# Performance work log

Hardware: AMD Instinct MI355X
Metric: run time of the kernel (lower is better)

The kernel has to match this reference:

```python
import jax, jax.numpy as jnp
import numpy as np

B, N, T = 1, 1024, 2048   # batch, graph nodes, timesteps
E, K = 16384, 32          # edges, causal kernel taps


def setup_inputs() -> dict:
    key = jax.random.key(0)
    k1, k2, k3, k4 = jax.random.split(key, 4)
    x = jax.random.normal(k1, (B, N, T), dtype=jnp.float32)
    # per-edge causal impulse-response kernels (aggregator(g) output)
    kernel = jax.random.normal(k2, (E, K), dtype=jnp.float32) * 0.1
    src = jax.random.randint(k3, (E,), 0, N)
    dst = jax.random.randint(k4, (E,), 0, N)
    return {"x": x, "kernel": kernel, "src": src, "dst": dst}


def reference(x, kernel, src, dst):
    # Block-sparse causal conv over the edge list:
    #   y_e[b, t] = sum_k kernel[e, k] * x[b, src_e, t - k]   (causal)
    #   out[b, n, t] = x[b, n, t] + sum_{e: dst_e = n} y_e[b, t]
    # (residual applied because g.include_index_diag is False)
    xs = x[:, src, :]                      # [B, E, T] gather upstream signals
    rhs = kernel[:, None, ::-1]            # [E, 1, K] flipped -> true causal conv
    y = jax.lax.conv_general_dilated(
        xs, rhs,
        window_strides=(1,),
        padding=[(K - 1, 0)],              # left-pad: strictly causal
        dimension_numbers=("NCW", "OIW", "NCW"),
        feature_group_count=E,             # one independent kernel per edge
    )                                      # [B, E, T]
    agg = jax.ops.segment_sum(jnp.swapaxes(y, 0, 1), dst, num_segments=N)  # [N, B, T]
    return x + jnp.swapaxes(agg, 0, 1)     # [B, N, T]
```

## Files before the change

kernel.cpp:

```cpp
#include <hip/hip_runtime.h>
#include <hip/hip_bf16.h>

#define TT  2048
#define KK  32
#define NN  1024
#define EE  16384
#define CAP 64
#define RS  2080

typedef short short8 __attribute__((ext_vector_type(8)));
typedef float f32x4  __attribute__((ext_vector_type(4)));

__device__ short g_xbf[NN * RS];

__device__ __forceinline__ short f2bf(float f) {
    __hip_bfloat16 h = __float2bfloat16(f);
    return __builtin_bit_cast(short, h);
}

__device__ __forceinline__ void gload_lds16(const short* g, short* l) {
    __builtin_amdgcn_global_load_lds(
        (const __attribute__((address_space(1))) void*)(const void*)(g),
        (__attribute__((address_space(3))) void*)(void*)(l), 16, 0, 0);
}

__global__ __launch_bounds__(256) void cvt_kernel(const float* __restrict__ x,
                                                  int* __restrict__ cnt) {
    const int bid = blockIdx.x, tid = threadIdx.x;
    if (bid < NN) {
        const float4* xr = (const float4*)(x + (size_t)bid * TT);
        const float4 u = xr[2 * tid], v = xr[2 * tid + 1];
        short8 h;
        h[0]=f2bf(u.x); h[1]=f2bf(u.y); h[2]=f2bf(u.z); h[3]=f2bf(u.w);
        h[4]=f2bf(v.x); h[5]=f2bf(v.y); h[6]=f2bf(v.z); h[7]=f2bf(v.w);
        *(short8*)&g_xbf[(size_t)bid * RS + 32 + 8 * tid] = h;
        if (tid < 4) {
            short8 z; z[0]=0;z[1]=0;z[2]=0;z[3]=0;z[4]=0;z[5]=0;z[6]=0;z[7]=0;
            *(short8*)&g_xbf[(size_t)bid * RS + 8 * tid] = z;
        }
    } else {
        ((int4*)cnt)[tid] = make_int4(0, 0, 0, 0);
    }
}

__global__ __launch_bounds__(256) void csr_kernel(const int* __restrict__ src,
                                                  const int* __restrict__ dst,
                                                  int* __restrict__ cnt,
                                                  unsigned* __restrict__ slots) {
    const int e = blockIdx.x * 256 + threadIdx.x;
    const int d = dst[e];
    const int p = atomicAdd(&cnt[d], 1);
    if (p < CAP) slots[(size_t)d * CAP + p] = ((unsigned)src[e] << 14) | (unsigned)e;
}

__global__ __launch_bounds__(128, 2) void lti_kernel(
    const float*    __restrict__ x,
    const float*    __restrict__ kern,
    const int*      __restrict__ cnt,
    const unsigned* __restrict__ slots,
    float*          __restrict__ out)
{
    const int n   = blockIdx.x;
    const int tid = threadIdx.x;
    const int pw  = tid >> 6;
    const int ln  = tid & 63;
    const int c   = ln & 15, g = ln >> 4;
    const int D   = 16 * c + 8 * g;

    __shared__ __align__(16) short xs_all[2][3][RS];
    __shared__ __align__(16) short kt_all[2][8][72];
    __shared__ __align__(16) float red[TT];
    __shared__ unsigned bl[CAP];

    short (*xsb)[RS] = xs_all[pw];
    short (*kt)[72]  = kt_all[pw];

    short8 z8; z8[0]=0;z8[1]=0;z8[2]=0;z8[3]=0;z8[4]=0;z8[5]=0;z8[6]=0;z8[7]=0;

    {
        short8* kz = (short8*)&kt[0][0];
        kz[ln] = z8;
        if (ln < 8) kz[64 + ln] = z8;
    }
    if (tid < CAP) bl[tid] = slots[(size_t)n * CAP + tid];
    int L = cnt[n]; if (L > CAP) L = CAP;
    __syncthreads();

    const int M = (L - pw + 1) >> 1;
    #define IDX(I) (pw + 2 * (I))

    f32x4 acc[8];
    #pragma unroll
    for (int s = 0; s < 8; ++s) { acc[s][0]=0.f; acc[s][1]=0.f; acc[s][2]=0.f; acc[s][3]=0.f; }

    float4 tr0, tr1, tr2;

    const int a_ = c & 7;
    const int s1 = ((a_ + 1) & 7) + 15 - c + 8 * g;

    #define ISSUE(S, P)                                                                \
    {                                                                                  \
        const unsigned sv = bl[P];                                                     \
        const int e0 = __builtin_amdgcn_readfirstlane((int)(sv & 16383u));             \
        const int s0 = __builtin_amdgcn_readfirstlane((int)(sv >> 14));                \
        const short* rb = g_xbf + (size_t)s0 * RS;                                     \
        gload_lds16(rb + 8 * ln,        &xsb[S][0]);                                   \
        gload_lds16(rb + 8 * ln + 512,  &xsb[S][512]);                                 \
        gload_lds16(rb + 8 * ln + 1024, &xsb[S][1024]);                                \
        gload_lds16(rb + 8 * ln + 1536, &xsb[S][1536]);                                \
        if (ln < 4) gload_lds16(rb + 8 * ln + 2048, &xsb[S][2048]);                    \
        tr##S = *(const float4*)(kern + ((size_t)e0 << 5) + 4 * (ln & 7));             \
    }

    #define COMMIT(S)                                                                  \
    {                                                                                  \
        const int a2 = ln >> 3, pad = (a2 + 1) & 7, mb = 4 * (ln & 7);                 \
        kt[a2][pad + 47 - mb] = f2bf(tr##S.x);                                         \
        kt[a2][pad + 46 - mb] = f2bf(tr##S.y);                                         \
        kt[a2][pad + 45 - mb] = f2bf(tr##S.z);                                         \
        kt[a2][pad + 44 - mb] = f2bf(tr##S.w);                                         \
    }

    #define COMPUTE(S)                                                                 \
    {                                                                                  \
        const short8 b1 = *(const short8*)&kt[a_][s1];                                 \
        short8 b2 = *(const short8*)&kt[a_][s1 + 16];                                  \
        if (g < 2) b2 = z8;                              \
        _Pragma("unroll")                                                              \
        for (int s = 0; s < 8; ++s) {                                                  \
            const short8 a1  = *(const short8*)&xsb[S][256 * s + D];                   \
            const short8 a2v = *(const short8*)&xsb[S][256 * s + D + 16];              \
            acc[s] = __builtin_amdgcn_mfma_f32_16x16x32_bf16(a1,  b1, acc[s], 0,0,0);  \
            acc[s] = __builtin_amdgcn_mfma_f32_16x16x32_bf16(a2v, b2, acc[s], 0,0,0);  \
        }                                                                              \
    }

    #define BODY(SC, SN, I)                                                            \
    if ((I) < M) {                                                                     \
        __builtin_amdgcn_sched_barrier(0);                                             \
        if ((I) + 2 < M) ISSUE(SN, IDX((I) + 2));                                      \
        const int rem = M - (I);                                                       \
        if (rem >= 3)      { asm volatile("s_waitcnt vmcnt(12)" ::: "memory"); }       \
        else if (rem == 2) { asm volatile("s_waitcnt vmcnt(6)"  ::: "memory"); }       \
        else               { asm volatile("s_waitcnt vmcnt(0)"  ::: "memory"); }       \
        __builtin_amdgcn_sched_barrier(0);                                             \
        COMMIT(SC);                                                                    \
        COMPUTE(SC);                                                                   \
    }

    if (M > 0) ISSUE(0, IDX(0));
    if (M > 1) ISSUE(1, IDX(1));
    for (int i = 0; i < M; i += 3) {
        BODY(0, 2, i);
        BODY(1, 0, i + 1);
        BODY(2, 1, i + 2);
    }

    if (pw == 1) {
        #pragma unroll
        for (int s = 0; s < 8; ++s)
            #pragma unroll
            for (int qd = 0; qd < 4; ++qd)
                red[256 * s + 64 * g + 16 * qd + c] = acc[s][qd];
    }
    __syncthreads();
    if (pw == 0) {
        const float* xr  = x   + (size_t)n * TT;
        float*       orw = out + (size_t)n * TT;
        #pragma unroll
        for (int s = 0; s < 8; ++s) {
            #pragma unroll
            for (int qd = 0; qd < 4; ++qd) {
                const int ta = 256 * s + 64 * g + 16 * qd + c;
                orw[ta] = xr[ta] + acc[s][qd] + red[ta];
            }
        }
    }
    #undef IDX
    #undef ISSUE
    #undef COMMIT
    #undef COMPUTE
    #undef BODY
}

extern "C" void kernel_launch(void* const* d_in, const int* in_sizes, int n_in,
                              void* d_out, int out_size, void* d_ws, size_t ws_size,
                              hipStream_t stream) {
    const float* x    = (const float*)d_in[0];
    const float* kern = (const float*)d_in[1];
    const int*   src  = (const int*)d_in[2];
    const int*   dst  = (const int*)d_in[3];
    float*       out  = (float*)d_out;

    int*      cnt   = (int*)d_ws;
    unsigned* slots = (unsigned*)((char*)d_ws + 4096);

    cvt_kernel<<<dim3(NN + 1), dim3(256), 0, stream>>>(x, cnt);
    csr_kernel<<<dim3(EE / 256), dim3(256), 0, stream>>>(src, dst, cnt, slots);
    lti_kernel<<<dim3(NN), dim3(128), 0, stream>>>(x, kern, cnt, slots, out);
}
```

Baseline: 34.72 us.

## Quantize signals and kernels to int8 and use i8 MFMA with per-edge scales

Replaces the bf16 conversion of x with per-row symmetric int8 quantization, and quantizes each edge's kernel to int8 in the CSR build pass. A combined per-slot scale is precomputed. The conv now uses mfma_i32_16x16x32_i8 and rescales into float accumulators per edge. This halves the bytes gathered per edge and the LDS footprint, but adds per-edge int-to-float conversions and loses accuracy relative to bf16, which may exceed tolerance.

```diff
diff --git a/kernel.cpp b/kernel.cpp
--- a/kernel.cpp
+++ b/kernel.cpp
@@ -8,17 +8,14 @@
 #define CAP 64
 #define RS  2080
 
-typedef short short8 __attribute__((ext_vector_type(8)));
-typedef float f32x4  __attribute__((ext_vector_type(4)));
-
-__device__ short g_xbf[NN * RS];
-
-__device__ __forceinline__ short f2bf(float f) {
-    __hip_bfloat16 h = __float2bfloat16(f);
-    return __builtin_bit_cast(short, h);
-}
-
-__device__ __forceinline__ void gload_lds16(const short* g, short* l) {
+typedef int   int4v __attribute__((ext_vector_type(4)));
+typedef float f32x4 __attribute__((ext_vector_type(4)));
+
+__device__ __align__(16) char  g_xi8[NN * RS];
+__device__ __align__(16) char  g_ki8[EE * KK];
+__device__ float g_xs[NN];
+
+__device__ __forceinline__ void gload_lds16(const char* g, char* l) {
     __builtin_amdgcn_global_load_lds(
         (const __attribute__((address_space(1))) void*)(const void*)(g),
         (__attribute__((address_space(3))) void*)(void*)(l), 16, 0, 0);
@@ -27,37 +24,85 @@
 __global__ __launch_bounds__(256) void cvt_kernel(const float* __restrict__ x,
                                                   int* __restrict__ cnt) {
     const int bid = blockIdx.x, tid = threadIdx.x;
-    if (bid < NN) {
-        const float4* xr = (const float4*)(x + (size_t)bid * TT);
-        const float4 u = xr[2 * tid], v = xr[2 * tid + 1];
-        short8 h;
-        h[0]=f2bf(u.x); h[1]=f2bf(u.y); h[2]=f2bf(u.z); h[3]=f2bf(u.w);
-        h[4]=f2bf(v.x); h[5]=f2bf(v.y); h[6]=f2bf(v.z); h[7]=f2bf(v.w);
-        *(short8*)&g_xbf[(size_t)bid * RS + 32 + 8 * tid] = h;
-        if (tid < 4) {
-            short8 z; z[0]=0;z[1]=0;z[2]=0;z[3]=0;z[4]=0;z[5]=0;z[6]=0;z[7]=0;
-            *(short8*)&g_xbf[(size_t)bid * RS + 8 * tid] = z;
-        }
-    } else {
-        ((int4*)cnt)[tid] = make_int4(0, 0, 0, 0);
-    }
-}
-
-__global__ __launch_bounds__(256) void csr_kernel(const int* __restrict__ src,
+    if (bid == NN) { ((int4*)cnt)[tid] = make_int4(0, 0, 0, 0); return; }
+    __shared__ float wmax[4];
+    __shared__ float sinv[2];
+    const float4* xr = (const float4*)(x + (size_t)bid * TT);
+    const float4 u = xr[2 * tid], v = xr[2 * tid + 1];
+    float m = fmaxf(fmaxf(fmaxf(fabsf(u.x), fabsf(u.y)), fmaxf(fabsf(u.z), fabsf(u.w))),
+                    fmaxf(fmaxf(fabsf(v.x), fabsf(v.y)), fmaxf(fabsf(v.z), fabsf(v.w))));
+    #pragma unroll
+    for (int o = 32; o; o >>= 1) m = fmaxf(m, __shfl_xor(m, o));
+    if ((tid & 63) == 0) wmax[tid >> 6] = m;
+    __syncthreads();
+    if (tid == 0) {
+        float mx = fmaxf(fmaxf(wmax[0], wmax[1]), fmaxf(wmax[2], wmax[3]));
+        mx = fmaxf(mx, 1e-20f);
+        sinv[0] = mx / 127.0f;
+        sinv[1] = 127.0f / mx;
+        g_xs[bid] = mx / 127.0f;
+    }
+    __syncthreads();
+    const float inv = sinv[1];
+    long pk = 0;
+    #pragma unroll
+    for (int j = 0; j < 8; ++j) {
+        const float val = (j < 4) ? ((j == 0) ? u.x : (j == 1) ? u.y : (j == 2) ? u.z : u.w)
+                                  : ((j == 4) ? v.x : (j == 5) ? v.y : (j == 6) ? v.z : v.w);
+        int q = (int)rintf(val * inv);
+        q = (q > 127) ? 127 : (q < -127 ? -127 : q);
+        pk |= ((long)(unsigned char)(signed char)q) << (8 * j);
+    }
+    *(long*)&g_xi8[(size_t)bid * RS + 32 + 8 * tid] = pk;
+    if (tid < 4) *(long*)&g_xi8[(size_t)bid * RS + 8 * tid] = 0L;
+}
+
+__global__ __launch_bounds__(256) void csr_kernel(const float* __restrict__ kern,
+                                                  const int* __restrict__ src,
                                                   const int* __restrict__ dst,
                                                   int* __restrict__ cnt,
-                                                  unsigned* __restrict__ slots) {
+                                                  unsigned* __restrict__ slots,
+                                                  float* __restrict__ sscale) {
     const int e = blockIdx.x * 256 + threadIdx.x;
-    const int d = dst[e];
+    float kv[KK];
+    float mk = 0.f;
+    #pragma unroll
+    for (int u = 0; u < 8; ++u) {
+        const float4 t = *(const float4*)(kern + (size_t)e * KK + 4 * u);
+        kv[4*u+0] = t.x; kv[4*u+1] = t.y; kv[4*u+2] = t.z; kv[4*u+3] = t.w;
+        mk = fmaxf(mk, fmaxf(fmaxf(fabsf(t.x), fabsf(t.y)), fmaxf(fabsf(t.z), fabsf(t.w))));
+    }
+    mk = fmaxf(mk, 1e-20f);
+    const float sk  = mk / 127.0f;
+    const float inv = 127.0f / mk;
+    int pw[8];
+    #pragma unroll
+    for (int u = 0; u < 8; ++u) {
+        int w = 0;
+        #pragma unroll
+        for (int j = 0; j < 4; ++j) {
+            int q = (int)rintf(kv[4*u+j] * inv);
+            q = (q > 127) ? 127 : (q < -127 ? -127 : q);
+            w |= ((int)(unsigned char)(signed char)q) << (8 * j);
+        }
+        pw[u] = w;
+    }
+    int4* kb = (int4*)(g_ki8 + (size_t)e * KK);
+    kb[0] = make_int4(pw[0], pw[1], pw[2], pw[3]);
+    kb[1] = make_int4(pw[4], pw[5], pw[6], pw[7]);
+    const int d = dst[e], s = src[e];
     const int p = atomicAdd(&cnt[d], 1);
-    if (p < CAP) slots[(size_t)d * CAP + p] = ((unsigned)src[e] << 14) | (unsigned)e;
+    if (p < CAP) {
+        slots[(size_t)d * CAP + p]  = ((unsigned)s << 14) | (unsigned)e;
+        sscale[(size_t)d * CAP + p] = g_xs[s] * sk;
+    }
 }
 
 __global__ __launch_bounds__(128, 2) void lti_kernel(
     const float*    __restrict__ x,
-    const float*    __restrict__ kern,
     const int*      __restrict__ cnt,
     const unsigned* __restrict__ slots,
+    const float*    __restrict__ sscale,
     float*          __restrict__ out)
 {
     const int n   = blockIdx.x;
@@ -67,22 +112,22 @@
     const int c   = ln & 15, g = ln >> 4;
     const int D   = 16 * c + 8 * g;
 
-    __shared__ __align__(16) short xs_all[2][3][RS];
-    __shared__ __align__(16) short kt_all[2][8][72];
+    __shared__ __align__(16) char  xs_all[2][3][RS];
+    __shared__ __align__(16) char  kt_all[2][8][72];
     __shared__ __align__(16) float red[TT];
     __shared__ unsigned bl[CAP];
-
-    short (*xsb)[RS] = xs_all[pw];
-    short (*kt)[72]  = kt_all[pw];
-
-    short8 z8; z8[0]=0;z8[1]=0;z8[2]=0;z8[3]=0;z8[4]=0;z8[5]=0;z8[6]=0;z8[7]=0;
+    __shared__ float    bs[CAP];
+
+    char (*xsb)[RS] = xs_all[pw];
+    char (*kt)[72]  = kt_all[pw];
 
     {
-        short8* kz = (short8*)&kt[0][0];
-        kz[ln] = z8;
-        if (ln < 8) kz[64 + ln] = z8;
-    }
-    if (tid < CAP) bl[tid] = slots[(size_t)n * CAP + tid];
+        if (ln < 36) ((int4*)&kt[0][0])[ln] = make_int4(0, 0, 0, 0);
+    }
+    if (tid < CAP) {
+        bl[tid] = slots[(size_t)n * CAP + tid];
+        bs[tid] = sscale[(size_t)n * CAP + tid];
+    }
     int L = cnt[n]; if (L > CAP) L = CAP;
     __syncthreads();
 
@@ -93,7 +138,8 @@
     #pragma unroll
     for (int s = 0; s < 8; ++s) { acc[s][0]=0.f; acc[s][1]=0.f; acc[s][2]=0.f; acc[s][3]=0.f; }
 
-    float4 tr0, tr1, tr2;
+    int   tw0, tw1, tw2;
+    float sc0, sc1, sc2;
 
     const int a_ = c & 7;
     const int s1 = ((a_ + 1) & 7) + 15 - c + 8 * g;
@@ -103,35 +149,39 @@
         const unsigned sv = bl[P];                                                     \
         const int e0 = __builtin_amdgcn_readfirstlane((int)(sv & 16383u));             \
         const int s0 = __builtin_amdgcn_readfirstlane((int)(sv >> 14));                \
-        const short* rb = g_xbf + (size_t)s0 * RS;                                     \
-        gload_lds16(rb + 8 * ln,        &xsb[S][0]);                                   \
-        gload_lds16(rb + 8 * ln + 512,  &xsb[S][512]);                                 \
-        gload_lds16(rb + 8 * ln + 1024, &xsb[S][1024]);                                \
-        gload_lds16(rb + 8 * ln + 1536, &xsb[S][1536]);                                \
-        if (ln < 4) gload_lds16(rb + 8 * ln + 2048, &xsb[S][2048]);                    \
-        tr##S = *(const float4*)(kern + ((size_t)e0 << 5) + 4 * (ln & 7));             \
+        const char* rb = g_xi8 + (size_t)s0 * RS;                                      \
+        gload_lds16(rb + 16 * ln,        &xsb[S][0]);                                  \
+        gload_lds16(rb + 16 * ln + 1024, &xsb[S][1024]);                               \
+        if (ln < 2) gload_lds16(rb + 16 * ln + 2048, &xsb[S][2048]);                   \
+        tw##S = *(const int*)(g_ki8 + ((size_t)e0 << 5) + 4 * (ln & 7));               \
+        sc##S = bs[P];                                                                 \
     }
 
     #define COMMIT(S)                                                                  \
     {                                                                                  \
         const int a2 = ln >> 3, pad = (a2 + 1) & 7, mb = 4 * (ln & 7);                 \
-        kt[a2][pad + 47 - mb] = f2bf(tr##S.x);                                         \
-        kt[a2][pad + 46 - mb] = f2bf(tr##S.y);                                         \
-        kt[a2][pad + 45 - mb] = f2bf(tr##S.z);                                         \
-        kt[a2][pad + 44 - mb] = f2bf(tr##S.w);                                         \
+        kt[a2][pad + 47 - mb] = (char)(tw##S);                                         \
+        kt[a2][pad + 46 - mb] = (char)(tw##S >> 8);                                    \
+        kt[a2][pad + 45 - mb] = (char)(tw##S >> 16);                                   \
+        kt[a2][pad + 44 - mb] = (char)(tw##S >> 24);                                   \
     }
 
     #define COMPUTE(S)                                                                 \
     {                                                                                  \
-        const short8 b1 = *(const short8*)&kt[a_][s1];                                 \
-        short8 b2 = *(const short8*)&kt[a_][s1 + 16];                                  \
-        if (g < 2) b2 = z8;                              \
+        const long b1 = *(const long*)&kt[a_][s1];                                     \
+        const long b2 = (g < 2) ? 0L : *(const long*)&kt[a_][s1 + 16];                 \
+        const float scv = sc##S;                                                       \
         _Pragma("unroll")                                                              \
         for (int s = 0; s < 8; ++s) {                                                  \
-            const short8 a1  = *(const short8*)&xsb[S][256 * s + D];                   \
-            const short8 a2v = *(const short8*)&xsb[S][256 * s + D + 16];              \
-            acc[s] = __builtin_amdgcn_mfma_f32_16x16x32_bf16(a1,  b1, acc[s], 0,0,0);  \
-            acc[s] = __builtin_amdgcn_mfma_f32_16x16x32_bf16(a2v, b2, acc[s], 0,0,0);  \
+            const long a1  = *(const long*)&xsb[S][256 * s + D];                       \
+            const long a2v = *(const long*)&xsb[S][256 * s + D + 16];                  \
+            int4v ti = {0, 0, 0, 0};                                                   \
+            ti = __builtin_amdgcn_mfma_i32_16x16x32_i8(a1,  b1, ti, 0, 0, 0);          \
+            ti = __builtin_amdgcn_mfma_i32_16x16x32_i8(a2v, b2, ti, 0, 0, 0);          \
+            acc[s][0] += scv * (float)ti[0];                                           \
+            acc[s][1] += scv * (float)ti[1];                                           \
+            acc[s][2] += scv * (float)ti[2];                                           \
+            acc[s][3] += scv * (float)ti[3];                                           \
         }                                                                              \
     }
 
@@ -140,9 +190,9 @@
         __builtin_amdgcn_sched_barrier(0);                                             \
         if ((I) + 2 < M) ISSUE(SN, IDX((I) + 2));                                      \
         const int rem = M - (I);                                                       \
-        if (rem >= 3)      { asm volatile("s_waitcnt vmcnt(12)" ::: "memory"); }       \
-        else if (rem == 2) { asm volatile("s_waitcnt vmcnt(6)"  ::: "memory"); }       \
-        else               { asm volatile("s_waitcnt vmcnt(0)"  ::: "memory"); }       \
+        if (rem >= 3)      { asm volatile("s_waitcnt vmcnt(8)" ::: "memory"); }        \
+        else if (rem == 2) { asm volatile("s_waitcnt vmcnt(4)" ::: "memory"); }        \
+        else               { asm volatile("s_waitcnt vmcnt(0)" ::: "memory"); }        \
         __builtin_amdgcn_sched_barrier(0);                                             \
         COMMIT(SC);                                                                    \
         COMPUTE(SC);                                                                   \
@@ -192,10 +242,11 @@
     const int*   dst  = (const int*)d_in[3];
     float*       out  = (float*)d_out;
 
-    int*      cnt   = (int*)d_ws;
-    unsigned* slots = (unsigned*)((char*)d_ws + 4096);
+    int*      cnt    = (int*)d_ws;
+    unsigned* slots  = (unsigned*)((char*)d_ws + 4096);
+    float*    sscale = (float*)((char*)d_ws + 4096 + 262144);
 
     cvt_kernel<<<dim3(NN + 1), dim3(256), 0, stream>>>(x, cnt);
-    csr_kernel<<<dim3(EE / 256), dim3(256), 0, stream>>>(src, dst, cnt, slots);
-    lti_kernel<<<dim3(NN), dim3(128), 0, stream>>>(x, kern, cnt, slots, out);
-}
+    csr_kernel<<<dim3(EE / 256), dim3(256), 0, stream>>>(kern, src, dst, cnt, slots, sscale);
+    lti_kernel<<<dim3(NN), dim3(128), 0, stream>>>(x, cnt, slots, sscale, out);
+}
```

After: 35.01 us. Within noise of the previous version (+0.8%).
